# Kernel tuning notes

Measured on AMD Instinct MI355X. Metric: run time of the kernel, lower is better.

## Reference

```python
import math
import jax, jax.numpy as jnp
import numpy as np

HIDDEN = 2048
N_HEAD = 32
N_KV = 8
HEAD_DIM = HIDDEN // N_HEAD  # 64
B, S = 2, 2048


def setup_inputs() -> dict:
    key = jax.random.key(0)
    ks = jax.random.split(key, 9)
    sc_h = 1.0 / math.sqrt(HIDDEN)
    return {
        "X": jax.random.normal(ks[0], (B, S, HIDDEN), jnp.float32),
        "Wq": jax.random.normal(ks[1], (HIDDEN, HIDDEN), jnp.float32) * sc_h,
        "bq": jax.random.normal(ks[2], (HIDDEN,), jnp.float32) * 0.01,
        "Wk": jax.random.normal(ks[3], (N_KV * HEAD_DIM, HIDDEN), jnp.float32) * sc_h,
        "bk": jax.random.normal(ks[4], (N_KV * HEAD_DIM,), jnp.float32) * 0.01,
        "Wv": jax.random.normal(ks[5], (N_KV * HEAD_DIM, HIDDEN), jnp.float32) * sc_h,
        "bv": jax.random.normal(ks[6], (N_KV * HEAD_DIM,), jnp.float32) * 0.01,
        "Wo": jax.random.normal(ks[7], (HIDDEN, HIDDEN), jnp.float32) * sc_h,
        "bo": jax.random.normal(ks[8], (HIDDEN,), jnp.float32) * 0.01,
    }


def reference(X, Wq, bq, Wk, bk, Wv, bv, Wo, bo):
    b, s, _ = X.shape
    g = N_HEAD // N_KV  # query heads per kv head (repeat_interleave group)
    scale = 1.0 / math.sqrt(HEAD_DIM)

    q = X @ Wq.T + bq                       # [B,S,H*D]
    k = X @ Wk.T + bk                       # [B,S,KV*D]
    v = X @ Wv.T + bv                       # [B,S,KV*D]

    # q grouped as (B, KV, g, S, D): head h = kv*g + j matches repeat_interleave on dim=1
    q = q.reshape(b, s, N_KV, g, HEAD_DIM).transpose(0, 2, 3, 1, 4)  # [B,KV,g,S,D]
    k = k.reshape(b, s, N_KV, HEAD_DIM).transpose(0, 2, 1, 3)         # [B,KV,S,D]
    v = v.reshape(b, s, N_KV, HEAD_DIM).transpose(0, 2, 1, 3)         # [B,KV,S,D]

    # scores without materializing repeated K/V: broadcast kv head over g query heads
    scores = jnp.einsum("bkgqd,bkld->bkgql", q, k) * scale            # [B,KV,g,S,S]
    weights = jax.nn.softmax(scores, axis=-1)
    out = jnp.einsum("bkgql,bkld->bkgqd", weights, v)                 # [B,KV,g,S,D]

    # replicate torch's contiguous .view(B, seq, -1) applied to the [B,H,S,D]
    # tensor WITHOUT transposing back: plain row-major reshape of (B,H,S,D).
    out = out.reshape(b, s, N_HEAD * HEAD_DIM)
    return out @ Wo.T + bo
```

## Files before the change

### kernel.cpp

```cpp
#include <hip/hip_runtime.h>

#define HIDDEN 2048
#define NHEADS 32
#define NKV    8
#define HDIM   64
#define BATCH  2
#define SEQ    2048
#define MROWS  (BATCH*SEQ)
#define NQKV   3072

#define SCALEQ 0.18033688011112042f

typedef _Float16 half8_t __attribute__((ext_vector_type(8)));
typedef _Float16 half4_t __attribute__((ext_vector_type(4)));
typedef __fp16   fp16x2_t __attribute__((ext_vector_type(2)));
typedef float    f32x4_t __attribute__((ext_vector_type(4)));

#define AS1 __attribute__((address_space(1)))
#define AS3 __attribute__((address_space(3)))

__device__ __forceinline__ void async_copy16(void* lds, const void* g) {
    __builtin_amdgcn_global_load_lds((AS1 void*)g, (AS3 void*)lds, 16, 0, 0);
}

#define PRIO1 __builtin_amdgcn_s_setprio(1)
#define PRIO0 __builtin_amdgcn_s_setprio(0)
#define BAR   __builtin_amdgcn_s_barrier()


#define QSTG_A(bi, u, kb) \
    async_copy16(&As[bi][(u)*4096 + ldst], Ag + (size_t)((u)*64) * 2048 + (kb))
#define QSTG_B(bi, u, kb) \
    async_copy16(&Bs[bi][(u)*4096 + ldst], Bg + (size_t)((u)*64) * 2048 + (kb))

__global__ __launch_bounds__(512, 4) void gemm_qkv(
    const _Float16* __restrict__ A, const _Float16* __restrict__ Bm,
    const float* __restrict__ bias, _Float16* __restrict__ Qb,
    _Float16* __restrict__ kfb, _Float16* __restrict__ vfb) {
    __shared__ _Float16 As[2][8192];
    __shared__ _Float16 Bs[2][12288];

    const int tid  = threadIdx.x;
    const int wave = tid >> 6;
    const int lane = tid & 63;
    const int quad = lane >> 4;
    const int l16  = lane & 15;
    const int wr   = wave >> 2;
    const int wc   = wave & 3;

    const int lin = (int)(blockIdx.y * gridDim.x + blockIdx.x);
    const int idx = (lin & 7) * 64 + (lin >> 3);
    const int m0  = (idx >> 4) * 128;
    const int n0  = (idx & 15) * 192;

    const int srow = tid >> 3;
    const int sg   = ((tid & 7) ^ (srow & 7)) << 3;
    const _Float16* Ag = A  + (size_t)(m0 + srow) * 2048 + sg;
    const _Float16* Bg = Bm + (size_t)(n0 + srow) * 2048 + sg;
    const int ldst = wave * 512;

    const int sk = l16 & 7;
    const int g0 = ((0 + quad) ^ sk) << 3;
    const int g1 = ((4 + quad) ^ sk) << 3;
    const int abase = wr * 4096 + l16 * 64;
    const int bbase = wc * 3072 + l16 * 64;

    f32x4_t acc[4][3] = {};

    QSTG_A(0, 0, 0);  QSTG_A(0, 1, 0);
    QSTG_B(0, 0, 0);  QSTG_B(0, 1, 0);  QSTG_B(0, 2, 0);
    QSTG_B(1, 0, 64); QSTG_B(1, 1, 64); QSTG_B(1, 2, 64);
    asm volatile("s_waitcnt vmcnt(3)" ::: "memory");
    BAR;

    for (int t = 0; t < 32; ++t) {
        const int  cur = t & 1;
        const int  kA  = (t + 1) << 6;
        const int  kB  = (t + 2) << 6;
        const bool sA  = (t + 1 < 32);
        const bool sB  = (t + 2 < 32);
        half8_t a[2][2], b[3][2];

#pragma unroll
        for (int mi = 0; mi < 2; ++mi) {
            a[mi][0] = *(const half8_t*)(&As[cur][abase + mi * 1024 + g0]);
            a[mi][1] = *(const half8_t*)(&As[cur][abase + mi * 1024 + g1]);
        }
#pragma unroll
        for (int ni = 0; ni < 3; ++ni) {
            b[ni][0] = *(const half8_t*)(&Bs[cur][bbase + ni * 1024 + g0]);
            b[ni][1] = *(const half8_t*)(&Bs[cur][bbase + ni * 1024 + g1]);
        }
        if (sA) { QSTG_A(cur ^ 1, 0, kA); QSTG_A(cur ^ 1, 1, kA); }
        BAR;
        PRIO1;
#pragma unroll
        for (int mi = 0; mi < 2; ++mi)
#pragma unroll
            for (int ni = 0; ni < 3; ++ni) {
                acc[mi][ni] = __builtin_amdgcn_mfma_f32_16x16x32_f16(a[mi][0], b[ni][0], acc[mi][ni], 0, 0, 0);
                acc[mi][ni] = __builtin_amdgcn_mfma_f32_16x16x32_f16(a[mi][1], b[ni][1], acc[mi][ni], 0, 0, 0);
            }
        PRIO0;
        BAR;
#pragma unroll
        for (int mi = 0; mi < 2; ++mi) {
            a[mi][0] = *(const half8_t*)(&As[cur][abase + (2 + mi) * 1024 + g0]);
            a[mi][1] = *(const half8_t*)(&As[cur][abase + (2 + mi) * 1024 + g1]);
        }
        if (sB) { QSTG_B(cur, 0, kB); QSTG_B(cur, 1, kB); QSTG_B(cur, 2, kB); }
        BAR;
        PRIO1;
#pragma unroll
        for (int mi = 0; mi < 2; ++mi)
#pragma unroll
            for (int ni = 0; ni < 3; ++ni) {
                acc[2 + mi][ni] = __builtin_amdgcn_mfma_f32_16x16x32_f16(a[mi][0], b[ni][0], acc[2 + mi][ni], 0, 0, 0);
                acc[2 + mi][ni] = __builtin_amdgcn_mfma_f32_16x16x32_f16(a[mi][1], b[ni][1], acc[2 + mi][ni], 0, 0, 0);
            }
        PRIO0;
        if (sB) { asm volatile("s_waitcnt vmcnt(3)" ::: "memory"); }
        else    { asm volatile("s_waitcnt vmcnt(0)" ::: "memory"); }
        BAR;
    }

#pragma unroll
    for (int ni = 0; ni < 3; ++ni) {
        const int cbase = n0 + wc * 48 + ni * 16;
        const int c  = cbase + l16;
        const float bv = bias[c];
        if (cbase < 2048) {
#pragma unroll
            for (int mi = 0; mi < 4; ++mi) {
                const int r0 = m0 + wr * 64 + mi * 16 + quad * 4;
#pragma unroll
                for (int i = 0; i < 4; ++i)
                    Qb[(size_t)(r0 + i) * HIDDEN + c] = (_Float16)(acc[mi][ni][i] + bv);
            }
        } else if (cbase < 2560) {
            const int kd = c - 2048;
            const int kvh = kd >> 6, d = kd & 63;
#pragma unroll
            for (int mi = 0; mi < 4; ++mi) {
                const int r0   = m0 + wr * 64 + mi * 16 + quad * 4;
                const int bb   = r0 >> 11;
                const int sblk = (r0 & 2047) >> 6;
                const int nt   = (r0 >> 4) & 3;
                _Float16* dst = kfb + ((size_t)(bb * 8 + kvh) * 32 + sblk) * 4096 +
                    ((nt * 2 + (d >> 5)) * 64 + ((d >> 3) & 3) * 16 + quad * 4) * 8 +
                    (d & 7);
#pragma unroll
                for (int i = 0; i < 4; ++i)
                    dst[i * 8] = (_Float16)(acc[mi][ni][i] + bv);
            }
        } else {
            const int kd = c - 2560;
            const int kvh = kd >> 6, d = kd & 63;
            const int dt = (d >> 4) & 3;
#pragma unroll
            for (int mi = 0; mi < 4; ++mi) {
                const int r0   = m0 + wr * 64 + mi * 16 + quad * 4;
                const int bb   = r0 >> 11;
                const int sblk = (r0 & 2047) >> 6;
                const int nt   = (r0 >> 4) & 3;
                half4_t h;
#pragma unroll
                for (int i = 0; i < 4; ++i) h[i] = (_Float16)(acc[mi][ni][i] + bv);
                *(half4_t*)(vfb + ((size_t)(bb * 8 + kvh) * 32 + sblk) * 4096 +
                            (nt * 2 + (dt >> 1)) * 512 + quad * 128 +
                            (d & 15) * 8 + (dt & 1) * 4) = h;
            }
        }
    }
}

#define OSTG_A(bi, u, kb) \
    async_copy16(&As[bi][(u)*4096 + ldst], Ag + (size_t)((u)*64) * 2048 + (kb))
#define OSTG_B(bi, u, kb) \
    async_copy16(&Bs[bi][(u)*4096 + ldst], Bg + (size_t)((u)*64) * 2048 + (kb))

__global__ __launch_bounds__(512, 4) void gemm_out(
    const _Float16* __restrict__ A, const _Float16* __restrict__ Bm,
    const float* __restrict__ bias, float* __restrict__ C) {
    __shared__ _Float16 As[2][8192];
    __shared__ _Float16 Bs[2][8192];

    const int tid  = threadIdx.x;
    const int wave = tid >> 6;
    const int lane = tid & 63;
    const int quad = lane >> 4;
    const int l16  = lane & 15;
    const int wr   = wave >> 2;
    const int wc   = wave & 3;

    const int lin = (int)(blockIdx.y * gridDim.x + blockIdx.x);
    const int idx = (lin & 7) * 64 + (lin >> 3);
    const int m0  = (idx >> 4) * 128;
    const int n0  = (idx & 15) * 128;

    const int srow = tid >> 3;
    const int sg   = ((tid & 7) ^ (srow & 7)) << 3;
    const _Float16* Ag = A  + (size_t)(m0 + srow) * 2048 + sg;
    const _Float16* Bg = Bm + (size_t)(n0 + srow) * 2048 + sg;
    const int ldst = wave * 512;

    const int sk = l16 & 7;
    const int g0 = ((0 + quad) ^ sk) << 3;
    const int g1 = ((4 + quad) ^ sk) << 3;
    const int abase = wr * 4096 + l16 * 64;
    const int bbase = wc * 2048 + l16 * 64;

    f32x4_t acc[4][2] = {};

    OSTG_A(0, 0, 0);  OSTG_A(0, 1, 0);
    OSTG_B(0, 0, 0);  OSTG_B(0, 1, 0);
    OSTG_B(1, 0, 64); OSTG_B(1, 1, 64);
    asm volatile("s_waitcnt vmcnt(2)" ::: "memory");
    BAR;

    for (int t = 0; t < 32; ++t) {
        const int  cur = t & 1;
        const int  kA  = (t + 1) << 6;
        const int  kB  = (t + 2) << 6;
        const bool sA  = (t + 1 < 32);
        const bool sB  = (t + 2 < 32);
        half8_t a[2][2], b[2][2];

#pragma unroll
        for (int mi = 0; mi < 2; ++mi) {
            a[mi][0] = *(const half8_t*)(&As[cur][abase + mi * 1024 + g0]);
            a[mi][1] = *(const half8_t*)(&As[cur][abase + mi * 1024 + g1]);
        }
#pragma unroll
        for (int ni = 0; ni < 2; ++ni) {
            b[ni][0] = *(const half8_t*)(&Bs[cur][bbase + ni * 1024 + g0]);
            b[ni][1] = *(const half8_t*)(&Bs[cur][bbase + ni * 1024 + g1]);
        }
        if (sA) { OSTG_A(cur ^ 1, 0, kA); OSTG_A(cur ^ 1, 1, kA); }
        BAR;
        PRIO1;
#pragma unroll
        for (int mi = 0; mi < 2; ++mi)
#pragma unroll
            for (int ni = 0; ni < 2; ++ni) {
                acc[mi][ni] = __builtin_amdgcn_mfma_f32_16x16x32_f16(a[mi][0], b[ni][0], acc[mi][ni], 0, 0, 0);
                acc[mi][ni] = __builtin_amdgcn_mfma_f32_16x16x32_f16(a[mi][1], b[ni][1], acc[mi][ni], 0, 0, 0);
            }
        PRIO0;
        BAR;
#pragma unroll
        for (int mi = 0; mi < 2; ++mi) {
            a[mi][0] = *(const half8_t*)(&As[cur][abase + (2 + mi) * 1024 + g0]);
            a[mi][1] = *(const half8_t*)(&As[cur][abase + (2 + mi) * 1024 + g1]);
        }
        if (sB) { OSTG_B(cur, 0, kB); OSTG_B(cur, 1, kB); }
        BAR;
        PRIO1;
#pragma unroll
        for (int mi = 0; mi < 2; ++mi)
#pragma unroll
            for (int ni = 0; ni < 2; ++ni) {
                acc[2 + mi][ni] = __builtin_amdgcn_mfma_f32_16x16x32_f16(a[mi][0], b[ni][0], acc[2 + mi][ni], 0, 0, 0);
                acc[2 + mi][ni] = __builtin_amdgcn_mfma_f32_16x16x32_f16(a[mi][1], b[ni][1], acc[2 + mi][ni], 0, 0, 0);
            }
        PRIO0;
        if (sB) { asm volatile("s_waitcnt vmcnt(2)" ::: "memory"); }
        else    { asm volatile("s_waitcnt vmcnt(0)" ::: "memory"); }
        BAR;
    }

#pragma unroll
    for (int ni = 0; ni < 2; ++ni) {
        const int c = n0 + wc * 32 + ni * 16 + l16;
        const float bv = bias[c];
#pragma unroll
        for (int mi = 0; mi < 4; ++mi) {
            const int r0 = m0 + wr * 64 + mi * 16 + quad * 4;
#pragma unroll
            for (int i = 0; i < 4; ++i)
                C[(size_t)(r0 + i) * HIDDEN + c] = acc[mi][ni][i] + bv;
        }
    }
}

__global__ __launch_bounds__(512, 8) void attn_kernel(
    const _Float16* __restrict__ Qb, const _Float16* __restrict__ Kf,
    const _Float16* __restrict__ Vf, _Float16* __restrict__ ctx) {
    __shared__ _Float16 S[16384];

    const int tid  = threadIdx.x;
    const int wave = tid >> 6;
    const int lane = tid & 63;
    const int quad = lane >> 4;
    const int l16  = lane & 15;
    const int qh   = wave >> 2;
    const int wh   = wave & 3;
    const int qt  = blockIdx.x;
    const int bkv = blockIdx.y;
    const int b   = bkv >> 3;
    const int kv  = bkv & 7;
    const int h   = kv * 4 + wh;

    const _Float16* qp = Qb +
        ((size_t)(b * SEQ + qt * 32 + qh * 16 + l16)) * HIDDEN + h * 64 + quad * 8;
    const half8_t qa0 = *(const half8_t*)qp;
    const half8_t qa1 = *(const half8_t*)(qp + 32);

    f32x4_t ot[4] = {};
    float fl = 0.f;

    const size_t kvbase = (size_t)(b * 8 + kv) * 32 * 4096;
    const int sh = wave * 512 + lane * 8;

    async_copy16(&S[wave * 512],        Kf + kvbase + sh);
    async_copy16(&S[8192 + wave * 512], Vf + kvbase + sh);

    for (int kt = 0; kt < SEQ / 64; ++kt) {
        __syncthreads();
        const int cur = kt & 1;
        if (kt + 1 < SEQ / 64) {
            const size_t off = kvbase + (size_t)(kt + 1) * 4096 + sh;
            async_copy16(&S[(cur ^ 1) * 4096 + wave * 512],        Kf + off);
            async_copy16(&S[8192 + (cur ^ 1) * 4096 + wave * 512], Vf + off);
        }
        const int kb = cur * 4096, vb = 8192 + cur * 4096;

#pragma unroll
        for (int nt = 0; nt < 4; ++nt) {
            const half8_t kf0 = *(const half8_t*)(&S[kb + ((nt * 2 + 0) * 64 + lane) * 8]);
            const half8_t kf1 = *(const half8_t*)(&S[kb + ((nt * 2 + 1) * 64 + lane) * 8]);
            f32x4_t s = {};
            s = __builtin_amdgcn_mfma_f32_16x16x32_f16(kf0, qa0, s, 0, 0, 0);
            s = __builtin_amdgcn_mfma_f32_16x16x32_f16(kf1, qa1, s, 0, 0, 0);
            const float e0 = __builtin_amdgcn_exp2f(s[0]);
            const float e1 = __builtin_amdgcn_exp2f(s[1]);
            const float e2 = __builtin_amdgcn_exp2f(s[2]);
            const float e3 = __builtin_amdgcn_exp2f(s[3]);
            fl += (e0 + e1) + (e2 + e3);
            const fp16x2_t lo = __builtin_amdgcn_cvt_pkrtz(e0, e1);
            const fp16x2_t hi = __builtin_amdgcn_cvt_pkrtz(e2, e3);
            half4_t p;
            p[0] = (_Float16)lo[0]; p[1] = (_Float16)lo[1];
            p[2] = (_Float16)hi[0]; p[3] = (_Float16)hi[1];
#pragma unroll
            for (int dp = 0; dp < 2; ++dp) {
                const half8_t vv = *(const half8_t*)(&S[vb + ((nt * 2 + dp) * 64 + lane) * 8]);
                const half4_t vlo = {vv[0], vv[1], vv[2], vv[3]};
                const half4_t vhi = {vv[4], vv[5], vv[6], vv[7]};
                ot[dp * 2]     = __builtin_amdgcn_mfma_f32_16x16x16f16(vlo, p, ot[dp * 2], 0, 0, 0);
                ot[dp * 2 + 1] = __builtin_amdgcn_mfma_f32_16x16x16f16(vhi, p, ot[dp * 2 + 1], 0, 0, 0);
            }
        }
    }

    fl += __shfl_xor(fl, 16);
    fl += __shfl_xor(fl, 32);

    __syncthreads();
    _Float16* T = S + wave * 1152;
    const float inv = 1.f / fl;
#pragma unroll
    for (int dt = 0; dt < 4; ++dt) {
        half4_t hh;
#pragma unroll
        for (int r = 0; r < 4; ++r) hh[r] = (_Float16)(ot[dt][r] * inv);
        *(half4_t*)(T + l16 * 72 + dt * 16 + quad * 4) = hh;
    }
    __builtin_amdgcn_s_waitcnt(0);
    _Float16* cp = ctx +
        (((size_t)b * 32 + h) * SEQ + qt * 32 + qh * 16 + l16) * 64;
#pragma unroll
    for (int pass = 0; pass < 2; ++pass) {
        const half8_t row = *(const half8_t*)(T + l16 * 72 + pass * 32 + quad * 8);
        *(half8_t*)(cp + pass * 32 + quad * 8) = row;
    }
}

__device__ __forceinline__ void cast4(const float* __restrict__ s,
                                      _Float16* __restrict__ d, int i, float sc) {
    const f32x4_t v = ((const f32x4_t*)s)[i];
    half4_t h;
#pragma unroll
    for (int j = 0; j < 4; ++j) h[j] = (_Float16)(v[j] * sc);
    ((half4_t*)d)[i] = h;
}

__global__ __launch_bounds__(256) void prep(
    const float* __restrict__ X,  const float* __restrict__ Wq,
    const float* __restrict__ Wk, const float* __restrict__ Wv,
    const float* __restrict__ Wo, const float* __restrict__ bq,
    const float* __restrict__ bk, const float* __restrict__ bv,
    _Float16* __restrict__ Xh, _Float16* __restrict__ Wqkv,
    _Float16* __restrict__ Woh, float* __restrict__ bqkv) {
    const int bid = blockIdx.x, tid = threadIdx.x;
    if (bid < 8192)       cast4(X,  Xh,   bid * 256 + tid, 1.f);
    else if (bid < 12288) cast4(Wq, Wqkv, (bid - 8192) * 256 + tid, SCALEQ);
    else if (bid < 13312) cast4(Wk, Wqkv + (size_t)HIDDEN * HIDDEN, (bid - 12288) * 256 + tid, 1.f);
    else if (bid < 14336) cast4(Wv, Wqkv + (size_t)(HIDDEN + 512) * HIDDEN, (bid - 13312) * 256 + tid, 1.f);
    else if (bid < 18432) cast4(Wo, Woh,  (bid - 14336) * 256 + tid, 1.f);
    else {
        const int i = (bid - 18432) * 256 + tid;
        if (i < 2048)      bqkv[i] = bq[i] * SCALEQ;
        else if (i < 2560) bqkv[i] = bk[i - 2048];
        else if (i < 3072) bqkv[i] = bv[i - 2560];
    }
}

extern "C" void kernel_launch(void* const* d_in, const int* in_sizes, int n_in,
                              void* d_out, int out_size, void* d_ws, size_t ws_size,
                              hipStream_t stream) {
    const float* X  = (const float*)d_in[0];
    const float* Wq = (const float*)d_in[1];
    const float* bq = (const float*)d_in[2];
    const float* Wk = (const float*)d_in[3];
    const float* bk = (const float*)d_in[4];
    const float* Wv = (const float*)d_in[5];
    const float* bv = (const float*)d_in[6];
    const float* Wo = (const float*)d_in[7];
    const float* bo = (const float*)d_in[8];
    float* out = (float*)d_out;

    char* p = (char*)d_ws;
    _Float16* Xh   = (_Float16*)p; p += (size_t)MROWS * HIDDEN * 2;
    _Float16* Wqkv = (_Float16*)p; p += (size_t)NQKV * HIDDEN * 2;
    _Float16* Woh  = (_Float16*)p; p += (size_t)HIDDEN * HIDDEN * 2;
    float*    bqkv = (float*)p;    p += (size_t)NQKV * 4;
    _Float16* Qb   = (_Float16*)p; p += (size_t)MROWS * HIDDEN * 2;
    _Float16* Kfb  = (_Float16*)p; p += (size_t)16 * 32 * 4096 * 2;
    _Float16* Vfb  = (_Float16*)p; p += (size_t)16 * 32 * 4096 * 2;
    _Float16* ctx  = Xh;

    prep<<<18444, 256, 0, stream>>>(X, Wq, Wk, Wv, Wo, bq, bk, bv,
                                    Xh, Wqkv, Woh, bqkv);

    gemm_qkv<<<dim3(NQKV / 192, MROWS / 128), 512, 0, stream>>>(
        Xh, Wqkv, bqkv, Qb, Kfb, Vfb);

    attn_kernel<<<dim3(SEQ / 32, BATCH * NKV), 512, 0, stream>>>(Qb, Kfb, Vfb, ctx);

    gemm_out<<<dim3(HIDDEN / 128, MROWS / 128), 512, 0, stream>>>(
        ctx, Woh, bo, out);
}
```

Baseline: 293.3 us.

## Process two query groups per wave in attention to reuse K/V tiles

Each attention block now covers 64 query rows instead of 32. Each wave handles two 16-row query groups against the same K/V LDS tile, which halves K/V global loads and LDS reads per query. The V layout written by the QKV GEMM changes to a half4 fragment order so V fragments load directly without splitting half8 vectors. The row-sum is now computed with an MFMA against a ones vector instead of scalar adds and shuffles. The cost is more registers per wave (occupancy hint lowered to 4) and half as many blocks in the grid.

```diff
diff --git a/kernel.cpp b/kernel.cpp
--- a/kernel.cpp
+++ b/kernel.cpp
@@ -167,8 +167,7 @@
 #pragma unroll
                 for (int i = 0; i < 4; ++i) h[i] = (_Float16)(acc[mi][ni][i] + bv);
                 *(half4_t*)(vfb + ((size_t)(bb * 8 + kvh) * 32 + sblk) * 4096 +
-                            (nt * 2 + (dt >> 1)) * 512 + quad * 128 +
-                            (d & 15) * 8 + (dt & 1) * 4) = h;
+                            ((nt * 4 + dt) * 64 + quad * 16 + (d & 15)) * 4) = h;
             }
         }
     }
@@ -283,17 +282,18 @@
     }
 }
 
-__global__ __launch_bounds__(512, 8) void attn_kernel(
+__global__ __launch_bounds__(512, 4) void attn_kernel(
     const _Float16* __restrict__ Qb, const _Float16* __restrict__ Kf,
     const _Float16* __restrict__ Vf, _Float16* __restrict__ ctx) {
-    __shared__ _Float16 S[16384];
+    __shared__ _Float16 Ks[2][4096];
+    __shared__ _Float16 Vs[2][4096];
 
     const int tid  = threadIdx.x;
     const int wave = tid >> 6;
     const int lane = tid & 63;
     const int quad = lane >> 4;
     const int l16  = lane & 15;
-    const int qh   = wave >> 2;
+    const int qs   = wave >> 2;
     const int wh   = wave & 3;
     const int qt  = blockIdx.x;
     const int bkv = blockIdx.y;
@@ -301,78 +301,85 @@
     const int kv  = bkv & 7;
     const int h   = kv * 4 + wh;
 
-    const _Float16* qp = Qb +
-        ((size_t)(b * SEQ + qt * 32 + qh * 16 + l16)) * HIDDEN + h * 64 + quad * 8;
-    const half8_t qa0 = *(const half8_t*)qp;
-    const half8_t qa1 = *(const half8_t*)(qp + 32);
-
-    f32x4_t ot[4] = {};
-    float fl = 0.f;
+    half8_t qa[2][2];
+#pragma unroll
+    for (int g = 0; g < 2; ++g) {
+        const _Float16* qp = Qb +
+            ((size_t)(b * SEQ + qt * 64 + qs * 32 + g * 16 + l16)) * HIDDEN +
+            h * 64 + quad * 8;
+        qa[g][0] = *(const half8_t*)qp;
+        qa[g][1] = *(const half8_t*)(qp + 32);
+    }
+
+    f32x4_t ot[2][4] = {};
+    f32x4_t lacc[2] = {};
+    const half4_t ones = {(_Float16)1.f, (_Float16)1.f, (_Float16)1.f, (_Float16)1.f};
 
     const size_t kvbase = (size_t)(b * 8 + kv) * 32 * 4096;
     const int sh = wave * 512 + lane * 8;
 
-    async_copy16(&S[wave * 512],        Kf + kvbase + sh);
-    async_copy16(&S[8192 + wave * 512], Vf + kvbase + sh);
+    async_copy16(&Ks[0][wave * 512], Kf + kvbase + sh);
+    async_copy16(&Vs[0][wave * 512], Vf + kvbase + sh);
 
     for (int kt = 0; kt < SEQ / 64; ++kt) {
         __syncthreads();
         const int cur = kt & 1;
         if (kt + 1 < SEQ / 64) {
             const size_t off = kvbase + (size_t)(kt + 1) * 4096 + sh;
-            async_copy16(&S[(cur ^ 1) * 4096 + wave * 512],        Kf + off);
-            async_copy16(&S[8192 + (cur ^ 1) * 4096 + wave * 512], Vf + off);
-        }
-        const int kb = cur * 4096, vb = 8192 + cur * 4096;
+            async_copy16(&Ks[cur ^ 1][wave * 512], Kf + off);
+            async_copy16(&Vs[cur ^ 1][wave * 512], Vf + off);
+        }
 
 #pragma unroll
         for (int nt = 0; nt < 4; ++nt) {
-            const half8_t kf0 = *(const half8_t*)(&S[kb + ((nt * 2 + 0) * 64 + lane) * 8]);
-            const half8_t kf1 = *(const half8_t*)(&S[kb + ((nt * 2 + 1) * 64 + lane) * 8]);
-            f32x4_t s = {};
-            s = __builtin_amdgcn_mfma_f32_16x16x32_f16(kf0, qa0, s, 0, 0, 0);
-            s = __builtin_amdgcn_mfma_f32_16x16x32_f16(kf1, qa1, s, 0, 0, 0);
-            const float e0 = __builtin_amdgcn_exp2f(s[0]);
-            const float e1 = __builtin_amdgcn_exp2f(s[1]);
-            const float e2 = __builtin_amdgcn_exp2f(s[2]);
-            const float e3 = __builtin_amdgcn_exp2f(s[3]);
-            fl += (e0 + e1) + (e2 + e3);
-            const fp16x2_t lo = __builtin_amdgcn_cvt_pkrtz(e0, e1);
-            const fp16x2_t hi = __builtin_amdgcn_cvt_pkrtz(e2, e3);
-            half4_t p;
-            p[0] = (_Float16)lo[0]; p[1] = (_Float16)lo[1];
-            p[2] = (_Float16)hi[0]; p[3] = (_Float16)hi[1];
-#pragma unroll
-            for (int dp = 0; dp < 2; ++dp) {
-                const half8_t vv = *(const half8_t*)(&S[vb + ((nt * 2 + dp) * 64 + lane) * 8]);
-                const half4_t vlo = {vv[0], vv[1], vv[2], vv[3]};
-                const half4_t vhi = {vv[4], vv[5], vv[6], vv[7]};
-                ot[dp * 2]     = __builtin_amdgcn_mfma_f32_16x16x16f16(vlo, p, ot[dp * 2], 0, 0, 0);
-                ot[dp * 2 + 1] = __builtin_amdgcn_mfma_f32_16x16x16f16(vhi, p, ot[dp * 2 + 1], 0, 0, 0);
-            }
-        }
-    }
-
-    fl += __shfl_xor(fl, 16);
-    fl += __shfl_xor(fl, 32);
+            const half8_t kf0 = *(const half8_t*)(&Ks[cur][((nt * 2 + 0) * 64 + lane) * 8]);
+            const half8_t kf1 = *(const half8_t*)(&Ks[cur][((nt * 2 + 1) * 64 + lane) * 8]);
+            half4_t p[2];
+#pragma unroll
+            for (int g = 0; g < 2; ++g) {
+                f32x4_t s = {};
+                s = __builtin_amdgcn_mfma_f32_16x16x32_f16(kf0, qa[g][0], s, 0, 0, 0);
+                s = __builtin_amdgcn_mfma_f32_16x16x32_f16(kf1, qa[g][1], s, 0, 0, 0);
+                const fp16x2_t lo = __builtin_amdgcn_cvt_pkrtz(
+                    __builtin_amdgcn_exp2f(s[0]), __builtin_amdgcn_exp2f(s[1]));
+                const fp16x2_t hi = __builtin_amdgcn_cvt_pkrtz(
+                    __builtin_amdgcn_exp2f(s[2]), __builtin_amdgcn_exp2f(s[3]));
+                half4_t pv;
+                pv[0] = (_Float16)lo[0]; pv[1] = (_Float16)lo[1];
+                pv[2] = (_Float16)hi[0]; pv[3] = (_Float16)hi[1];
+                p[g] = pv;
+                lacc[g] = __builtin_amdgcn_mfma_f32_16x16x16f16(ones, pv, lacc[g], 0, 0, 0);
+            }
+#pragma unroll
+            for (int dt = 0; dt < 4; ++dt) {
+                const half4_t vf = *(const half4_t*)(&Vs[cur][((nt * 4 + dt) * 64 + lane) * 4]);
+                ot[0][dt] = __builtin_amdgcn_mfma_f32_16x16x16f16(vf, p[0], ot[0][dt], 0, 0, 0);
+                ot[1][dt] = __builtin_amdgcn_mfma_f32_16x16x16f16(vf, p[1], ot[1][dt], 0, 0, 0);
+            }
+        }
+    }
 
     __syncthreads();
-    _Float16* T = S + wave * 1152;
-    const float inv = 1.f / fl;
-#pragma unroll
-    for (int dt = 0; dt < 4; ++dt) {
-        half4_t hh;
-#pragma unroll
-        for (int r = 0; r < 4; ++r) hh[r] = (_Float16)(ot[dt][r] * inv);
-        *(half4_t*)(T + l16 * 72 + dt * 16 + quad * 4) = hh;
-    }
-    __builtin_amdgcn_s_waitcnt(0);
-    _Float16* cp = ctx +
-        (((size_t)b * 32 + h) * SEQ + qt * 32 + qh * 16 + l16) * 64;
-#pragma unroll
-    for (int pass = 0; pass < 2; ++pass) {
-        const half8_t row = *(const half8_t*)(T + l16 * 72 + pass * 32 + quad * 8);
-        *(half8_t*)(cp + pass * 32 + quad * 8) = row;
+    _Float16* T = &Ks[0][0] + wave * 1152;
+#pragma unroll
+    for (int g = 0; g < 2; ++g) {
+        const float inv = 1.f / lacc[g][0];
+#pragma unroll
+        for (int dt = 0; dt < 4; ++dt) {
+            half4_t hh;
+#pragma unroll
+            for (int r = 0; r < 4; ++r) hh[r] = (_Float16)(ot[g][dt][r] * inv);
+            *(half4_t*)(T + l16 * 72 + dt * 16 + quad * 4) = hh;
+        }
+        __builtin_amdgcn_s_waitcnt(0);
+        _Float16* cp = ctx +
+            (((size_t)b * 32 + h) * SEQ + qt * 64 + qs * 32 + g * 16 + l16) * 64;
+#pragma unroll
+        for (int pass = 0; pass < 2; ++pass) {
+            const half8_t row = *(const half8_t*)(T + l16 * 72 + pass * 32 + quad * 8);
+            *(half8_t*)(cp + pass * 32 + quad * 8) = row;
+        }
+        __builtin_amdgcn_s_waitcnt(0);
     }
 }
 
@@ -436,7 +443,7 @@
     gemm_qkv<<<dim3(NQKV / 192, MROWS / 128), 512, 0, stream>>>(
         Xh, Wqkv, bqkv, Qb, Kfb, Vfb);
 
-    attn_kernel<<<dim3(SEQ / 32, BATCH * NKV), 512, 0, stream>>>(Qb, Kfb, Vfb, ctx);
+    attn_kernel<<<dim3(SEQ / 64, BATCH * NKV), 512, 0, stream>>>(Qb, Kfb, Vfb, ctx);
 
     gemm_out<<<dim3(HIDDEN / 128, MROWS / 128), 512, 0, stream>>>(
         ctx, Woh, bo, out);
```

New measurement: 293.9 us (median of 2 runs). No clear change (+0.2%).
